# Kernel tuning notes

Measured on AMD Instinct MI355X. Metric: run time of the kernel, lower is better.

## Reference

```python
import jax, jax.numpy as jnp
import numpy as np

B, N, S = 8, 16384, 2048
C1, C2 = 128, 256
MLP = [256, 256]
BN_EPS = 1e-5


def setup_inputs() -> dict:
    key = jax.random.key(0)
    ks = jax.random.split(key, 12)
    inp = {
        "xyz1": jax.random.normal(ks[0], (B, N, 3), dtype=jnp.float32),
        "xyz2": jax.random.normal(ks[1], (B, S, 3), dtype=jnp.float32),
        "points1": jax.random.normal(ks[2], (B, C1, N), dtype=jnp.float32),
        "points2": jax.random.normal(ks[3], (B, C2, S), dtype=jnp.float32),
    }
    cin = C1 + C2
    kidx = 4
    for li, cout in enumerate(MLP):
        inp[f"W{li}"] = jax.random.normal(ks[kidx], (cout, cin), dtype=jnp.float32) * (1.0 / np.sqrt(cin))
        inp[f"b{li}"] = jnp.zeros((cout,), dtype=jnp.float32)
        inp[f"g{li}"] = jnp.ones((cout,), dtype=jnp.float32)
        inp[f"beta{li}"] = jnp.zeros((cout,), dtype=jnp.float32)
        cin = cout
        kidx += 1
    return inp


def _interpolate(xyz1, xyz2, points2):
    # D[b,n,s] = ||xyz1[b,n] - xyz2[b,s]||^2
    D = jnp.sum((xyz1[:, :, None, :] - xyz2[:, None, :, :]) ** 2, axis=-1)  # [B,N,S]
    neg_dist, idx = jax.lax.top_k(-D, 3)  # 3 smallest distances, ascending
    dist = jnp.maximum(-neg_dist, 1e-10)  # [B,N,3]
    w = 1.0 / dist
    weight = w / jnp.sum(w, axis=2, keepdims=True)  # [B,N,3]
    p2 = jnp.transpose(points2, (0, 2, 1))  # [B,S,C2]
    gathered = p2[jnp.arange(p2.shape[0])[:, None, None], idx]  # [B,N,3,C2]
    return jnp.einsum("bnkc,bnk->bcn", gathered, weight)  # [B,C2,N]


def _conv_bn_relu(x, W, b, g, beta):
    # 1x1 conv over points: [B,Cin,N] -> [B,Cout,N]
    y = jnp.einsum("oc,bcn->bon", W, x) + b[None, :, None]
    mean = jnp.mean(y, axis=(0, 2), keepdims=True)
    var = jnp.var(y, axis=(0, 2), keepdims=True)  # biased, training-mode BN
    yh = (y - mean) * jax.lax.rsqrt(var + BN_EPS)
    return jax.nn.relu(yh * g[None, :, None] + beta[None, :, None])


def reference(xyz1, xyz2, points1, points2, W0, b0, g0, beta0, W1, b1, g1, beta1):
    interp = _interpolate(xyz1, xyz2, points2)  # [B,C2,N]
    h = jnp.concatenate([interp, points1], axis=1)  # [B,C1+C2,N]
    h = _conv_bn_relu(h, W0, b0, g0, beta0)
    h = _conv_bn_relu(h, W1, b1, g1, beta1)
    return h
```

## Files before the change

### kernel.cpp

```cpp
#include <hip/hip_runtime.h>
#include <hip/hip_bf16.h>


typedef unsigned int u32;
typedef unsigned short u16;
typedef unsigned long long u64;
typedef __attribute__((ext_vector_type(8))) short short8;
typedef __attribute__((ext_vector_type(4))) float f32x4;

#define NT_TOTAL 131072
#define NN 16384
#define SS 2048

__device__ __forceinline__ float bf2f(u16 u) {
    union { u32 i; float f; } cv; cv.i = ((u32)u) << 16; return cv.f;
}
__device__ __forceinline__ u16 f2bf(float f) {
    union { float f; u32 i; } cv; cv.f = f;
    const u32 r = (cv.i + 0x7FFFu + ((cv.i >> 16) & 1u)) >> 16;
    return (u16)r;
}
__device__ __forceinline__ float ldf(const void* p, int i, int isbf) {
    return isbf ? bf2f(((const u16*)p)[i]) : ((const float*)p)[i];
}

__global__ __launch_bounds__(256)
void detect_kernel(const u32* __restrict__ xyz1w, u32* __restrict__ flag,
                   float* __restrict__ stats)
{
    __shared__ int cnt;
    const int t = threadIdx.x;
    if (t == 0) cnt = 0;
    for (int i = t; i < 1024; i += 256) stats[i] = 0.f;
    __syncthreads();
    if (t < 64) {
        const u32 w = xyz1w[t];
        const int e = (int)((w >> 7) & 0xFF);
        if (e >= 96 && e <= 144) atomicAdd(&cnt, 1);
    }
    __syncthreads();
    if (t == 0) flag[0] = (cnt >= 48) ? 1u : 0u;
}

__global__ __launch_bounds__(256)
void sentinel_kernel(u16* __restrict__ out, int n)
{
    const int i = blockIdx.x * 256 + threadIdx.x;
    if (i < n) out[i] = 0x4496;
}

__global__ __launch_bounds__(256)
void param_kernel(const void* W0, const void* b0, const void* g0, const void* bt0,
                  const void* W1, const void* b1, const void* g1, const void* bt1,
                  const u32* __restrict__ flag,
                  u16* __restrict__ Wb0, u16* __restrict__ Wb1, float* __restrict__ pf)
{
    const int isbf = (int)flag[0];
    const int i = blockIdx.x * 256 + threadIdx.x;
    if (i < 98304) Wb0[i] = f2bf(ldf(W0, i, isbf));
    if (i < 65536) Wb1[i] = f2bf(ldf(W1, i, isbf));
    if (i < 1536) {
        const void* srcs[6] = { b0, g0, bt0, b1, g1, bt1 };
        pf[i] = ldf(srcs[i >> 8], i & 255, isbf);
    }
}

__global__ __launch_bounds__(256)
void pack2_kernel(const void* __restrict__ xyz2, float4* __restrict__ s2q,
                  const u32* __restrict__ flag)
{
    const int isbf = (int)flag[0];
    const int i = blockIdx.x * 256 + threadIdx.x;
    if (i < 8 * SS) {
        const float x = ldf(xyz2, i * 3 + 0, isbf);
        const float y = ldf(xyz2, i * 3 + 1, isbf);
        const float z = ldf(xyz2, i * 3 + 2, isbf);
        float4 v; v.x = x; v.y = y; v.z = z; v.w = x * x + y * y + z * z;
        s2q[i] = v;
    }
}

__global__ __launch_bounds__(256)
void transpose_kernel(const void* __restrict__ in, u16* __restrict__ out,
                      int Cc, int Np, int ldout, int coff, const u32* __restrict__ flag)
{
    __shared__ u16 tile[64][72];
    const int isbf = (int)flag[0];
    const int t = threadIdx.x;
    const int n0 = blockIdx.x * 64, c0 = blockIdx.y * 64, bz = blockIdx.z;
    const int ch = t & 7, r = t >> 3;
#pragma unroll
    for (int p = 0; p < 2; ++p) {
        const int cl = r + p * 32;
        const size_t idx = ((size_t)(bz * Cc + c0 + cl)) * Np + n0 + ch * 8;
        union { uint4 v; u16 us[8]; } pk;
        if (isbf) {
            pk.v = *(const uint4*)((const u16*)in + idx);
        } else {
            const float4 va = *(const float4*)((const float*)in + idx);
            const float4 vb = *(const float4*)((const float*)in + idx + 4);
            pk.us[0] = f2bf(va.x); pk.us[1] = f2bf(va.y);
            pk.us[2] = f2bf(va.z); pk.us[3] = f2bf(va.w);
            pk.us[4] = f2bf(vb.x); pk.us[5] = f2bf(vb.y);
            pk.us[6] = f2bf(vb.z); pk.us[7] = f2bf(vb.w);
        }
        *(uint4*)&tile[cl][ch * 8] = pk.v;
    }
    __syncthreads();
#pragma unroll
    for (int p = 0; p < 2; ++p) {
        const int nl = r + p * 32;
        union { uint4 v; u16 us[8]; } pk;
#pragma unroll
        for (int i = 0; i < 8; ++i) pk.us[i] = tile[ch * 8 + i][nl];
        *(uint4*)&out[((size_t)(bz * Np + n0 + nl)) * ldout + coff + c0 + ch * 8] = pk.v;
    }
}

__global__ __launch_bounds__(256)
void knn_kernel(const float4* __restrict__ s2q, const void* __restrict__ xyz1,
                u32* __restrict__ idxA, float* __restrict__ wA,
                const u32* __restrict__ flag)
{
    __shared__ float skeys[4][64][5];
    const int isbf = (int)flag[0];
    const int t = threadIdx.x;
    const int lane = t & 63;
    const int wid = __builtin_amdgcn_readfirstlane(t >> 6);
    const int qg = blockIdx.x * 64 + lane;
    const int b = blockIdx.x >> 8;
    const float qx = ldf(xyz1, qg * 3 + 0, isbf);
    const float qy = ldf(xyz1, qg * 3 + 1, isbf);
    const float qz = ldf(xyz1, qg * 3 + 2, isbf);
    const float qx2 = -2.f * qx, qy2 = -2.f * qy, qz2 = -2.f * qz;
    const float qc = qx * qx + qy * qy + qz * qz;
    const float4* __restrict__ S = s2q + (size_t)b * SS;

    float k0 = __builtin_inff(), k1 = k0, k2 = k0, k3 = k0, k4 = k0;
    const int sbase = wid * 512;
#pragma unroll 8
    for (int it = 0; it < 512; ++it) {
        const int s = sbase + it;
        const float4 v = S[s];
        float d = fmaf(v.x, qx2, qc);
        d = fmaf(v.y, qy2, d);
        d = fmaf(v.z, qz2, d);
        d += v.w;
        const float k = __uint_as_float((__float_as_uint(d) & 0xFFFFF800u) | (u32)s);
        const float o0 = fminf(k, k0);
        const float o1 = __builtin_amdgcn_fmed3f(k, k0, k1);
        const float o2 = __builtin_amdgcn_fmed3f(k, k1, k2);
        const float o3 = __builtin_amdgcn_fmed3f(k, k2, k3);
        const float o4 = __builtin_amdgcn_fmed3f(k, k3, k4);
        k0 = o0; k1 = o1; k2 = o2; k3 = o3; k4 = o4;
    }
    skeys[wid][lane][0] = k0;
    skeys[wid][lane][1] = k1;
    skeys[wid][lane][2] = k2;
    skeys[wid][lane][3] = k3;
    skeys[wid][lane][4] = k4;
    __syncthreads();
    if (wid != 0) return;

    u64 e0 = ~0ull, e1 = ~0ull, e2 = ~0ull;
#pragma unroll
    for (int w = 0; w < 4; ++w)
#pragma unroll
        for (int i = 0; i < 5; ++i) {
            const u32 idx = __float_as_uint(skeys[w][lane][i]) & 0x7FFu;
            const float4 c = S[idx];
            const float dx = qx - c.x, dy = qy - c.y, dz = qz - c.z;
            const float d = fmaf(dz, dz, fmaf(dy, dy, dx * dx));
            const u64 e = ((u64)__float_as_uint(d) << 11) | (u64)idx;
            const bool c0 = e < e0, c1 = e < e1, c2 = e < e2;
            e2 = c1 ? e1 : (c2 ? e : e2);
            e1 = c0 ? e0 : (c1 ? e : e1);
            e0 = c0 ? e : e0;
        }
    const u32 i0 = (u32)(e0 & 0x7FF), i1 = (u32)(e1 & 0x7FF), i2 = (u32)(e2 & 0x7FF);
    const float d0 = fmaxf(__uint_as_float((u32)(e0 >> 11)), 1e-10f);
    const float d1 = fmaxf(__uint_as_float((u32)(e1 >> 11)), 1e-10f);
    const float d2 = fmaxf(__uint_as_float((u32)(e2 >> 11)), 1e-10f);
    const float w0 = 1.f / d0, w1 = 1.f / d1, w2 = 1.f / d2;
    const float inv = 1.f / (w0 + w1 + w2);
    idxA[qg * 3 + 0] = i0; idxA[qg * 3 + 1] = i1; idxA[qg * 3 + 2] = i2;
    wA[qg * 3 + 0] = w0 * inv; wA[qg * 3 + 1] = w1 * inv; wA[qg * 3 + 2] = w2 * inv;
}

__global__ __launch_bounds__(256)
void interp_kernel(const u16* __restrict__ p2T, const u32* __restrict__ idxA,
                   const float* __restrict__ wA, u16* __restrict__ hT)
{
    const int t = threadIdx.x;
    const int pl = t >> 5, g = t & 31;
    const int qg = blockIdx.x * 8 + pl;
    const int b = qg >> 14;
    float acc[8] = {0.f, 0.f, 0.f, 0.f, 0.f, 0.f, 0.f, 0.f};
#pragma unroll
    for (int k = 0; k < 3; ++k) {
        const u32 idx = idxA[qg * 3 + k];
        const float w = wA[qg * 3 + k];
        union { uint4 v; u16 us[8]; } pk;
        pk.v = *(const uint4*)(p2T + ((size_t)(b * SS + idx)) * 256 + g * 8);
#pragma unroll
        for (int e = 0; e < 8; ++e) acc[e] = fmaf(w, bf2f(pk.us[e]), acc[e]);
    }
    union { uint4 v; u16 us[8]; } ov;
#pragma unroll
    for (int e = 0; e < 8; ++e) ov.us[e] = f2bf(acc[e]);
    *(uint4*)&hT[(size_t)qg * 384 + g * 8] = ov.v;
}

#define GEMM_BODY(BUF, OTH, KCUR)                                                        \
    {                                                                                    \
        short8 a[4], b[4];                                                               \
        _Pragma("unroll")                                                                \
        for (int i = 0; i < 4; ++i) a[i] = *(const short8*)&aT[BUF][aoff[i]];            \
        _Pragma("unroll")                                                                \
        for (int j = 0; j < 4; ++j) b[j] = *(const short8*)&bT[BUF][boff[j]];            \
        _Pragma("unroll")                                                                \
        for (int i = 0; i < 4; ++i)                                                      \
            _Pragma("unroll")                                                            \
            for (int j = 0; j < 4; ++j)                                                  \
                acc[i][j] = __builtin_amdgcn_mfma_f32_16x16x32_bf16(a[i], b[j], acc[i][j], 0, 0, 0); \
        if ((KCUR) + 32 < K) {                                                           \
            *(uint4*)&aT[OTH][o0] = ra0; *(uint4*)&aT[OTH][o1] = ra1;                    \
            *(uint4*)&bT[OTH][o0] = rb0; *(uint4*)&bT[OTH][o1] = rb1;                    \
            if ((KCUR) + 64 < K) {                                                       \
                ra0 = *(const uint4*)(gA0 + (KCUR) + 64);                                \
                ra1 = *(const uint4*)(gA1 + (KCUR) + 64);                                \
                rb0 = *(const uint4*)(gB0 + (KCUR) + 64);                                \
                rb1 = *(const uint4*)(gB1 + (KCUR) + 64);                                \
            }                                                                            \
        }                                                                                \
        __syncthreads();                                                                 \
    }

__global__ __launch_bounds__(256)
void gemm_kernel(const u16* __restrict__ A, const u16* __restrict__ Bm,
                 const float* __restrict__ bias, void* __restrict__ yout, int K,
                 const u32* __restrict__ flag,
                 float* __restrict__ sums, float* __restrict__ sumsq)
{
    __shared__ __align__(16) u16 aT[2][128 * 32];
    __shared__ __align__(16) u16 bT[2][128 * 32];
    const int isbf = (int)flag[0];
    const int t = threadIdx.x;
    const int lane = t & 63;
    const int l15 = lane & 15;
    const int q = lane >> 4;
    const int wid = t >> 6;
    const int n0 = blockIdx.x * 128;
    const int m0 = blockIdx.y * 128;
    const int wm = (wid & 1) * 64;
    const int wn = (wid >> 1) * 64;

    f32x4 acc[4][4] = {};

    const int ca0 = t, ca1 = t + 256;
    const u16* gA0 = A + (size_t)(m0 + (ca0 >> 2)) * K + (ca0 & 3) * 8;
    const u16* gA1 = A + (size_t)(m0 + (ca1 >> 2)) * K + (ca1 & 3) * 8;
    const u16* gB0 = Bm + (size_t)(n0 + (ca0 >> 2)) * K + (ca0 & 3) * 8;
    const u16* gB1 = Bm + (size_t)(n0 + (ca1 >> 2)) * K + (ca1 & 3) * 8;
    const int o0 = (ca0 >> 2) * 32 + (((ca0 & 3) ^ ((ca0 >> 3) & 3)) * 8);
    const int o1 = (ca1 >> 2) * 32 + (((ca1 & 3) ^ ((ca1 >> 3) & 3)) * 8);

    const int gsw = (l15 >> 1) & 3;
    int aoff[4], boff[4];
#pragma unroll
    for (int i = 0; i < 4; ++i) {
        aoff[i] = (wm + i * 16 + l15) * 32 + ((q ^ gsw) * 8);
        boff[i] = (wn + i * 16 + l15) * 32 + ((q ^ gsw) * 8);
    }

    uint4 ra0 = *(const uint4*)(gA0);
    uint4 ra1 = *(const uint4*)(gA1);
    uint4 rb0 = *(const uint4*)(gB0);
    uint4 rb1 = *(const uint4*)(gB1);
    *(uint4*)&aT[0][o0] = ra0; *(uint4*)&aT[0][o1] = ra1;
    *(uint4*)&bT[0][o0] = rb0; *(uint4*)&bT[0][o1] = rb1;
    ra0 = *(const uint4*)(gA0 + 32);
    ra1 = *(const uint4*)(gA1 + 32);
    rb0 = *(const uint4*)(gB0 + 32);
    rb1 = *(const uint4*)(gB1 + 32);
    __syncthreads();

    for (int kk = 0; kk < K; kk += 64) {
        GEMM_BODY(0, 1, kk)
        GEMM_BODY(1, 0, kk + 32)
    }

#pragma unroll
    for (int i = 0; i < 4; ++i) {
        const int mBase = m0 + wm + i * 16 + q * 4;
        float bi[4];
#pragma unroll
        for (int r = 0; r < 4; ++r) bi[r] = bias[mBase + r];
#pragma unroll
        for (int j = 0; j < 4; ++j) {
            const int col = n0 + wn + j * 16 + l15;
            const size_t obase = ((size_t)(col >> 14) * 256) * NN + (col & 16383);
#pragma unroll
            for (int r = 0; r < 4; ++r) {
                const float v = acc[i][j][r] + bi[r];
                const size_t oi = obase + (size_t)(mBase + r) * NN;
                if (isbf) ((u16*)yout)[oi] = f2bf(v);
                else      ((float*)yout)[oi] = v;
            }
        }
    }

    float* sds = (float*)&aT[0][0];
    const int wp = wid >> 1;
#pragma unroll
    for (int i = 0; i < 4; ++i) {
        const int mloc = wm + i * 16 + q * 4;
#pragma unroll
        for (int r = 0; r < 4; ++r) {
            const float bi = bias[m0 + mloc + r];
            float s = 0.f, sq = 0.f;
#pragma unroll
            for (int j = 0; j < 4; ++j) {
                const float v = acc[i][j][r] + bi;
                s += v; sq += v * v;
            }
#pragma unroll
            for (int off = 1; off < 16; off <<= 1) {
                s += __shfl_xor(s, off);
                sq += __shfl_xor(sq, off);
            }
            if (l15 == 0) {
                sds[wp * 128 + mloc + r] = s;
                sds[256 + wp * 128 + mloc + r] = sq;
            }
        }
    }
    __syncthreads();
    if (t < 128) {
        atomicAdd(&sums[m0 + t], sds[t] + sds[128 + t]);
    } else if (t < 256) {
        const int c = t - 128;
        atomicAdd(&sumsq[m0 + c], sds[256 + c] + sds[384 + c]);
    }
}

__global__ __launch_bounds__(256)
void bn_act_tr_kernel(const void* __restrict__ y, const float* __restrict__ sums,
                      const float* __restrict__ sumsq, const float* __restrict__ gam,
                      const float* __restrict__ beta, u16* __restrict__ h2,
                      const u32* __restrict__ flag)
{
    __shared__ u16 tile[64][68];
    const int isbf = (int)flag[0];
    const int t = threadIdx.x;
    const int n0g = blockIdx.x * 64, c0 = blockIdx.y * 64;
    const int bb = n0g >> 14, nn0 = n0g & 16383;
    const float invNT = 1.0f / (float)NT_TOTAL;
    {
        const int f4 = t & 15, cbase = t >> 4;
#pragma unroll
        for (int p = 0; p < 4; ++p) {
            const int cl = cbase + p * 16;
            const int c = c0 + cl;
            const float mean = sums[c] * invNT;
            const float var = sumsq[c] * invNT - mean * mean;
            const float rstd = rsqrtf(var + 1e-5f);
            const float sc = gam[c] * rstd;
            const float sh = beta[c] - mean * sc;
            const size_t base = ((size_t)(bb * 256 + c)) * NN + nn0 + f4 * 4;
            float in4[4];
            if (isbf) {
                union { uint2 v2; u16 us[4]; } iv;
                iv.v2 = *(const uint2*)((const u16*)y + base);
#pragma unroll
                for (int e = 0; e < 4; ++e) in4[e] = bf2f(iv.us[e]);
            } else {
                const float4 v = *(const float4*)((const float*)y + base);
                in4[0] = v.x; in4[1] = v.y; in4[2] = v.z; in4[3] = v.w;
            }
            union { uint2 v2; u16 us[4]; } o;
#pragma unroll
            for (int e = 0; e < 4; ++e) {
                float v = in4[e] * sc + sh;
                v = (v != v) ? 777.0f : fmaxf(v, 0.f);
                o.us[e] = f2bf(v);
            }
            *(uint2*)&tile[cl][f4 * 4] = o.v2;
        }
    }
    __syncthreads();
    {
        const int ch = t & 7, rr = t >> 3;
#pragma unroll
        for (int p = 0; p < 2; ++p) {
            const int nl = rr + p * 32;
            union { uint4 v; u16 us[8]; } pk;
#pragma unroll
            for (int i = 0; i < 8; ++i) pk.us[i] = tile[ch * 8 + i][nl];
            *(uint4*)&h2[((size_t)(n0g + nl)) * 256 + c0 + ch * 8] = pk.v;
        }
    }
}

__global__ __launch_bounds__(256)
void final_kernel(void* __restrict__ y, const float* __restrict__ sums,
                  const float* __restrict__ sumsq, const float* __restrict__ gam,
                  const float* __restrict__ beta, const u32* __restrict__ flag)
{
    const int isbf = (int)flag[0];
    const int gid = blockIdx.x * 256 + threadIdx.x;
    const int c = (gid >> 12) & 255;
    const float invNT = 1.0f / (float)NT_TOTAL;
    const float mean = sums[c] * invNT;
    const float var = sumsq[c] * invNT - mean * mean;
    const float rstd = rsqrtf(var + 1e-5f);
    const float sc = gam[c] * rstd;
    const float sh = beta[c] - mean * sc;
    const size_t idx4 = (size_t)gid * 4;
    float in4[4];
    if (isbf) {
        union { uint2 v2; u16 us[4]; } iv;
        iv.v2 = *(const uint2*)((const u16*)y + idx4);
#pragma unroll
        for (int e = 0; e < 4; ++e) in4[e] = bf2f(iv.us[e]);
    } else {
        const float4 v = *(const float4*)((const float*)y + idx4);
        in4[0] = v.x; in4[1] = v.y; in4[2] = v.z; in4[3] = v.w;
    }
    float o4[4];
#pragma unroll
    for (int e = 0; e < 4; ++e) {
        float v = in4[e] * sc + sh;
        o4[e] = (v != v) ? 777.0f : fmaxf(v, 0.f);
    }
    if (isbf) {
        union { uint2 v2; u16 us[4]; } o;
#pragma unroll
        for (int e = 0; e < 4; ++e) o.us[e] = f2bf(o4[e]);
        *(uint2*)((u16*)y + idx4) = o.v2;
    } else {
        float4 o; o.x = o4[0]; o.y = o4[1]; o.z = o4[2]; o.w = o4[3];
        *(float4*)((float*)y + idx4) = o;
    }
}

__global__ void pointnet_fp_module_24532853195517_kernel() {}

extern "C" void kernel_launch(void* const* d_in, const int* in_sizes, int n_in,
                              void* d_out, int out_size, void* d_ws, size_t ws_size,
                              hipStream_t stream)
{
    const void* xyz1    = d_in[0];
    const void* xyz2    = d_in[1];
    const void* points1 = d_in[2];
    const void* points2 = d_in[3];
    const void* W0 = d_in[4];  const void* b0 = d_in[5];
    const void* g0 = d_in[6];  const void* bt0 = d_in[7];
    const void* W1 = d_in[8];  const void* b1 = d_in[9];
    const void* g1 = d_in[10]; const void* bt1 = d_in[11];

    char* ws = (char*)d_ws;
    float* stats = (float*)ws;
    u32* flag    = (u32*)(ws + 4096);
    float* pf    = (float*)(ws + 8192);
    u16* Wb0     = (u16*)(ws + 16384);
    u16* Wb1     = (u16*)(ws + 212992);
    u32* idxA    = (u32*)(ws + 344064);
    float* wA    = (float*)(ws + 1916928);
    u16* p2T     = (u16*)(ws + 3489792);
    u16* hT      = (u16*)(ws + 11878400);
    u16* h2      = hT;
    float* sum0 = stats, *sq0 = stats + 256, *sum1 = stats + 512, *sq1 = stats + 768;

    float4* s2q = (float4*)((char*)d_out + (8u << 20));

    if (ws_size < (size_t)112541696) {
        sentinel_kernel<<<(out_size + 255) / 256, 256, 0, stream>>>((u16*)d_out, out_size);
        return;
    }

    sentinel_kernel<<<16, 256, 0, stream>>>((u16*)d_out, 4096);

    detect_kernel<<<1, 256, 0, stream>>>((const u32*)xyz1, flag, stats);
    param_kernel<<<384, 256, 0, stream>>>(W0, b0, g0, bt0, W1, b1, g1, bt1, flag, Wb0, Wb1, pf);
    pack2_kernel<<<64, 256, 0, stream>>>(xyz2, s2q, flag);
    transpose_kernel<<<dim3(32, 4, 8), 256, 0, stream>>>(points2, p2T, 256, 2048, 256, 0, flag);
    transpose_kernel<<<dim3(256, 2, 8), 256, 0, stream>>>(points1, hT, 128, 16384, 384, 256, flag);
    knn_kernel<<<2048, 256, 0, stream>>>(s2q, xyz1, idxA, wA, flag);
    interp_kernel<<<16384, 256, 0, stream>>>(p2T, idxA, wA, hT);
    gemm_kernel<<<dim3(1024, 2), 256, 0, stream>>>(Wb0, hT, pf + 0, d_out, 384, flag, sum0, sq0);
    bn_act_tr_kernel<<<dim3(2048, 4), 256, 0, stream>>>(d_out, sum0, sq0, pf + 256, pf + 512, h2, flag);
    gemm_kernel<<<dim3(1024, 2), 256, 0, stream>>>(Wb1, h2, pf + 768, d_out, 256, flag, sum1, sq1);
    final_kernel<<<32768, 256, 0, stream>>>(d_out, sum1, sq1, pf + 1024, pf + 1280, flag);
}
```

Measured before the change: 550.0 us.

## Write first GEMM output point-major bf16 via LDS, replace BN transpose with elementwise pass

The first GEMM now stages its tile in shared memory and writes bf16 output in point-major [N,256] layout with coalesced 16-byte stores. This lets the BN+ReLU step become a simple elementwise grid-stride kernel with per-channel scale and shift held in shared memory, replacing the transposing kernel. It removes the strided channel-major writes and the LDS transpose in the BN pass. In exchange it adds a larger LDS footprint and an extra sync in the GEMM epilogue, and the intermediate is always stored as bf16 regardless of the input dtype flag.

```diff
diff --git a/kernel.cpp b/kernel.cpp
--- a/kernel.cpp
+++ b/kernel.cpp
@@ -240,10 +240,13 @@
 void gemm_kernel(const u16* __restrict__ A, const u16* __restrict__ Bm,
                  const float* __restrict__ bias, void* __restrict__ yout, int K,
                  const u32* __restrict__ flag,
-                 float* __restrict__ sums, float* __restrict__ sumsq)
-{
-    __shared__ __align__(16) u16 aT[2][128 * 32];
-    __shared__ __align__(16) u16 bT[2][128 * 32];
+                 float* __restrict__ sums, float* __restrict__ sumsq, int outmode)
+{
+    __shared__ __align__(16) u16 lds[18432];
+    u16* const aT[2] = { lds, lds + 4096 };
+    u16* const bT[2] = { lds + 8192, lds + 12288 };
+    float* const sds = (float*)(lds + 17408);
+
     const int isbf = (int)flag[0];
     const int t = threadIdx.x;
     const int lane = t & 63;
@@ -254,6 +257,7 @@
     const int m0 = blockIdx.y * 128;
     const int wm = (wid & 1) * 64;
     const int wn = (wid >> 1) * 64;
+    const int wp = wid >> 1;
 
     f32x4 acc[4][4] = {};
 
@@ -290,6 +294,58 @@
         GEMM_BODY(1, 0, kk + 32)
     }
 
+    if (outmode) {
+#pragma unroll
+        for (int i = 0; i < 4; ++i) {
+            const int mloc = wm + i * 16 + q * 4;
+            float bi[4];
+#pragma unroll
+            for (int r = 0; r < 4; ++r) bi[r] = bias[m0 + mloc + r];
+#pragma unroll
+            for (int r = 0; r < 4; ++r) {
+                float s = 0.f, sq = 0.f;
+#pragma unroll
+                for (int j = 0; j < 4; ++j) {
+                    const float v = acc[i][j][r] + bi[r];
+                    s += v; sq += v * v;
+                }
+#pragma unroll
+                for (int off = 1; off < 16; off <<= 1) {
+                    s += __shfl_xor(s, off);
+                    sq += __shfl_xor(sq, off);
+                }
+                if (l15 == 0) {
+                    sds[wp * 128 + mloc + r] = s;
+                    sds[256 + wp * 128 + mloc + r] = sq;
+                }
+            }
+#pragma unroll
+            for (int j = 0; j < 4; ++j) {
+                const int nl = wn + j * 16 + l15;
+                union { u64 w; u16 us[4]; } pk;
+#pragma unroll
+                for (int r = 0; r < 4; ++r) pk.us[r] = f2bf(acc[i][j][r] + bi[r]);
+                *(u64*)&lds[nl * 136 + mloc] = pk.w;
+            }
+        }
+        __syncthreads();
+        u16* outp = (u16*)yout;
+#pragma unroll
+        for (int it = 0; it < 8; ++it) {
+            const int row = (t >> 4) + it * 16;
+            const int cc = (t & 15) * 8;
+            const uint4 v = *(const uint4*)&lds[row * 136 + cc];
+            *(uint4*)&outp[((size_t)(n0 + row)) * 256 + m0 + cc] = v;
+        }
+        if (t < 128) {
+            atomicAdd(&sums[m0 + t], sds[t] + sds[128 + t]);
+        } else if (t < 256) {
+            const int c = t - 128;
+            atomicAdd(&sumsq[m0 + c], sds[256 + c] + sds[384 + c]);
+        }
+        return;
+    }
+
 #pragma unroll
     for (int i = 0; i < 4; ++i) {
         const int mBase = m0 + wm + i * 16 + q * 4;
@@ -309,9 +365,6 @@
             }
         }
     }
-
-    float* sds = (float*)&aT[0][0];
-    const int wp = wid >> 1;
 #pragma unroll
     for (int i = 0; i < 4; ++i) {
         const int mloc = wm + i * 16 + q * 4;
@@ -345,60 +398,33 @@
 }
 
 __global__ __launch_bounds__(256)
-void bn_act_tr_kernel(const void* __restrict__ y, const float* __restrict__ sums,
-                      const float* __restrict__ sumsq, const float* __restrict__ gam,
-                      const float* __restrict__ beta, u16* __restrict__ h2,
-                      const u32* __restrict__ flag)
-{
-    __shared__ u16 tile[64][68];
-    const int isbf = (int)flag[0];
+void bn_elem_kernel(const u16* __restrict__ h0, const float* __restrict__ sums,
+                    const float* __restrict__ sumsq, const float* __restrict__ gam,
+                    const float* __restrict__ beta, u16* __restrict__ h2)
+{
+    __shared__ float ssc[256], ssh[256];
     const int t = threadIdx.x;
-    const int n0g = blockIdx.x * 64, c0 = blockIdx.y * 64;
-    const int bb = n0g >> 14, nn0 = n0g & 16383;
-    const float invNT = 1.0f / (float)NT_TOTAL;
     {
-        const int f4 = t & 15, cbase = t >> 4;
-#pragma unroll
-        for (int p = 0; p < 4; ++p) {
-            const int cl = cbase + p * 16;
-            const int c = c0 + cl;
-            const float mean = sums[c] * invNT;
-            const float var = sumsq[c] * invNT - mean * mean;
-            const float rstd = rsqrtf(var + 1e-5f);
-            const float sc = gam[c] * rstd;
-            const float sh = beta[c] - mean * sc;
-            const size_t base = ((size_t)(bb * 256 + c)) * NN + nn0 + f4 * 4;
-            float in4[4];
-            if (isbf) {
-                union { uint2 v2; u16 us[4]; } iv;
-                iv.v2 = *(const uint2*)((const u16*)y + base);
-#pragma unroll
-                for (int e = 0; e < 4; ++e) in4[e] = bf2f(iv.us[e]);
-            } else {
-                const float4 v = *(const float4*)((const float*)y + base);
-                in4[0] = v.x; in4[1] = v.y; in4[2] = v.z; in4[3] = v.w;
-            }
-            union { uint2 v2; u16 us[4]; } o;
-#pragma unroll
-            for (int e = 0; e < 4; ++e) {
-                float v = in4[e] * sc + sh;
-                v = (v != v) ? 777.0f : fmaxf(v, 0.f);
-                o.us[e] = f2bf(v);
-            }
-            *(uint2*)&tile[cl][f4 * 4] = o.v2;
-        }
-    }
-    __syncthreads();
-    {
-        const int ch = t & 7, rr = t >> 3;
-#pragma unroll
-        for (int p = 0; p < 2; ++p) {
-            const int nl = rr + p * 32;
-            union { uint4 v; u16 us[8]; } pk;
-#pragma unroll
-            for (int i = 0; i < 8; ++i) pk.us[i] = tile[ch * 8 + i][nl];
-            *(uint4*)&h2[((size_t)(n0g + nl)) * 256 + c0 + ch * 8] = pk.v;
-        }
+        const float invNT = 1.0f / (float)NT_TOTAL;
+        const float mean = sums[t] * invNT;
+        const float var = sumsq[t] * invNT - mean * mean;
+        const float rstd = rsqrtf(var + 1e-5f);
+        const float sc = gam[t] * rstd;
+        ssc[t] = sc;
+        ssh[t] = beta[t] - mean * sc;
+    }
+    __syncthreads();
+    for (u32 g = blockIdx.x * 256 + t; g < 4194304u; g += 4096u * 256u) {
+        const int cb = (g & 31) * 8;
+        union { uint4 v; u16 us[8]; } iv, ov;
+        iv.v = *(const uint4*)(h0 + (size_t)g * 8);
+#pragma unroll
+        for (int e = 0; e < 8; ++e) {
+            float v = bf2f(iv.us[e]) * ssc[cb + e] + ssh[cb + e];
+            v = (v != v) ? 777.0f : fmaxf(v, 0.f);
+            ov.us[e] = f2bf(v);
+        }
+        *(uint4*)(h2 + (size_t)g * 8) = ov.v;
     }
 }
 
@@ -472,6 +498,7 @@
     u16* h2      = hT;
     float* sum0 = stats, *sq0 = stats + 256, *sum1 = stats + 512, *sq1 = stats + 768;
 
+    u16* h0 = (u16*)d_out;
     float4* s2q = (float4*)((char*)d_out + (8u << 20));
 
     if (ws_size < (size_t)112541696) {
@@ -488,8 +515,8 @@
     transpose_kernel<<<dim3(256, 2, 8), 256, 0, stream>>>(points1, hT, 128, 16384, 384, 256, flag);
     knn_kernel<<<2048, 256, 0, stream>>>(s2q, xyz1, idxA, wA, flag);
     interp_kernel<<<16384, 256, 0, stream>>>(p2T, idxA, wA, hT);
-    gemm_kernel<<<dim3(1024, 2), 256, 0, stream>>>(Wb0, hT, pf + 0, d_out, 384, flag, sum0, sq0);
-    bn_act_tr_kernel<<<dim3(2048, 4), 256, 0, stream>>>(d_out, sum0, sq0, pf + 256, pf + 512, h2, flag);
-    gemm_kernel<<<dim3(1024, 2), 256, 0, stream>>>(Wb1, h2, pf + 768, d_out, 256, flag, sum1, sq1);
+    gemm_kernel<<<dim3(1024, 2), 256, 0, stream>>>(Wb0, hT, pf + 0, h0, 384, flag, sum0, sq0, 1);
+    bn_elem_kernel<<<4096, 256, 0, stream>>>(h0, sum0, sq0, pf + 256, pf + 512, h2);
+    gemm_kernel<<<dim3(1024, 2), 256, 0, stream>>>(Wb1, h2, pf + 768, d_out, 256, flag, sum1, sq1, 0);
     final_kernel<<<32768, 256, 0, stream>>>(d_out, sum1, sq1, pf + 1024, pf + 1280, flag);
 }
```

New measurement: 534.4 us. 2.8% less time.
